# Kernel optimization log

Measured on AMD Instinct MI355X. Metric: run time of the kernel, lower is better.

The kernel has to match this reference:

```python
import jax, jax.numpy as jnp
import numpy as np

EMBED = 768
HIDDEN = 4 * EMBED
TEMPERATURE = 1.0
LN_EPS = 1e-5


def setup_inputs() -> dict:
    key = jax.random.key(0)
    ks = jax.random.split(key, 10)
    s = 1.0 / np.sqrt(EMBED)
    sh = 1.0 / np.sqrt(HIDDEN)
    return {
        "x": jax.random.normal(ks[0], (32, 577, EMBED), dtype=jnp.float32),
        "Wq": jax.random.normal(ks[1], (EMBED, EMBED), dtype=jnp.float32) * s,
        "Wk": jax.random.normal(ks[2], (EMBED, EMBED), dtype=jnp.float32) * s,
        "Wv": jax.random.normal(ks[3], (EMBED, EMBED), dtype=jnp.float32) * s,
        "ln1_g": jnp.ones((EMBED,), jnp.float32),
        "ln1_b": jnp.zeros((EMBED,), jnp.float32),
        "ln2_g": jnp.ones((EMBED,), jnp.float32),
        "ln2_b": jnp.zeros((EMBED,), jnp.float32),
        "W1": jax.random.normal(ks[4], (EMBED, HIDDEN), dtype=jnp.float32) * s,
        "b1": jnp.zeros((HIDDEN,), jnp.float32),
        "W2": jax.random.normal(ks[5], (HIDDEN, EMBED), dtype=jnp.float32) * sh,
        "b2": jnp.zeros((EMBED,), jnp.float32),
    }


def layer_norm(x, g, b):
    mu = jnp.mean(x, axis=-1, keepdims=True)
    var = jnp.mean(jnp.square(x - mu), axis=-1, keepdims=True)
    return (x - mu) * jax.lax.rsqrt(var + LN_EPS) * g + b


def l2_attention(h, Wq, Wk, Wv):
    # h: [b, s, d]
    Q = h @ Wq
    K = h @ Wk
    V = h @ Wv
    q_sq = jnp.sum(Q * Q, axis=-1, keepdims=True)          # [b, s, 1]
    k_sq = jnp.sum(K * K, axis=-1, keepdims=True)          # [b, s, 1]
    qk = jnp.einsum('bqd,bkd->bqk', Q, K)                  # [b, s, s]
    l2_sq = q_sq + jnp.swapaxes(k_sq, -2, -1) - 2.0 * qk
    attn = jax.nn.softmax(-l2_sq / TEMPERATURE, axis=-1)
    return jnp.einsum('bqk,bkd->bqd', attn, V)


def reference(x, Wq, Wk, Wv, ln1_g, ln1_b, ln2_g, ln2_b, W1, b1, W2, b2):
    x = x + l2_attention(layer_norm(x, ln1_g, ln1_b), Wq, Wk, Wv)
    h = layer_norm(x, ln2_g, ln2_b)
    h = jax.nn.gelu(h @ W1 + b1, approximate=False) @ W2 + b2
    return x + h
```

## Files before the change

### kernel.cpp

```cpp
#include <hip/hip_runtime.h>

#define EMBED 768
#define HIDDEN 3072
#define SEQ 577
#define BATCH 32
#define ROWS (BATCH*SEQ)
#define KPAD 608
#define SLD 640

typedef __attribute__((ext_vector_type(4))) float f32x4;
typedef __attribute__((ext_vector_type(8))) __bf16 bf16x8;
typedef unsigned int __attribute__((address_space(1))) as1_u32;
typedef unsigned int __attribute__((address_space(3))) as3_u32;

__device__ __forceinline__ unsigned short f2b(float f) {
    unsigned int u = __float_as_uint(f);
    u = u + 0x7FFFu + ((u >> 16) & 1u);
    return (unsigned short)(u >> 16);
}
__device__ __forceinline__ float b2f(unsigned short s) {
    return __uint_as_float(((unsigned int)s) << 16);
}
__device__ __forceinline__ void gld16(const unsigned short* g, unsigned short* l) {
    __builtin_amdgcn_global_load_lds((const as1_u32*)g, (as3_u32*)l, 16, 0, 0);
}
__device__ __forceinline__ float gelu_f(float x) {
    float u = x * (0.7978845608028654f + 0.03567740814183f * x * x);
    float e = __expf(2.0f * u);
    float th = 1.0f - 2.0f / (e + 1.0f);
    return 0.5f * x * (1.0f + th);
}

__device__ __forceinline__ int swz_lin() {
    int nx = gridDim.x;
    int lin = blockIdx.y * nx + blockIdx.x;
    if (gridDim.z == 1) {
        int nwg = nx * gridDim.y;
        int q = nwg >> 3, r = nwg & 7;
        int xcd = lin & 7, blk = lin >> 3;
        lin = (xcd < r ? xcd * (q + 1) : r * (q + 1) + (xcd - r) * q) + blk;
    }
    return lin;
}

__global__ void ln_kernel(const float* __restrict__ x, const float* __restrict__ g,
                          const float* __restrict__ b, unsigned short* __restrict__ o) {
    int row = blockIdx.x;
    const float* xr = x + (size_t)row * EMBED;
    int t = threadIdx.x;
    float v0 = xr[t], v1 = xr[t + 256], v2 = xr[t + 512];
    float s = v0 + v1 + v2;
    float ss = v0 * v0 + v1 * v1 + v2 * v2;
#pragma unroll
    for (int d = 32; d; d >>= 1) { s += __shfl_down(s, d); ss += __shfl_down(ss, d); }
    __shared__ float rs[4], rss[4];
    if ((t & 63) == 0) { rs[t >> 6] = s; rss[t >> 6] = ss; }
    __syncthreads();
    s = rs[0] + rs[1] + rs[2] + rs[3];
    ss = rss[0] + rss[1] + rss[2] + rss[3];
    float mu = s * (1.0f / EMBED);
    float var = ss * (1.0f / EMBED) - mu * mu;
    float rstd = rsqrtf(var + 1e-5f);
    unsigned short* orow = o + (size_t)row * EMBED;
    orow[t]       = f2b((v0 - mu) * rstd * g[t]       + b[t]);
    orow[t + 256] = f2b((v1 - mu) * rstd * g[t + 256] + b[t + 256]);
    orow[t + 512] = f2b((v2 - mu) * rstd * g[t + 512] + b[t + 512]);
}

__global__ void ln_split_kernel(const float* __restrict__ x, const float* __restrict__ g,
                                const float* __restrict__ b, unsigned short* __restrict__ oh,
                                unsigned short* __restrict__ ol) {
    int row = blockIdx.x;
    const float* xr = x + (size_t)row * EMBED;
    int t = threadIdx.x;
    float v0 = xr[t], v1 = xr[t + 256], v2 = xr[t + 512];
    float s = v0 + v1 + v2;
    float ss = v0 * v0 + v1 * v1 + v2 * v2;
#pragma unroll
    for (int d = 32; d; d >>= 1) { s += __shfl_down(s, d); ss += __shfl_down(ss, d); }
    __shared__ float rs[4], rss[4];
    if ((t & 63) == 0) { rs[t >> 6] = s; rss[t >> 6] = ss; }
    __syncthreads();
    s = rs[0] + rs[1] + rs[2] + rs[3];
    ss = rss[0] + rss[1] + rss[2] + rss[3];
    float mu = s * (1.0f / EMBED);
    float var = ss * (1.0f / EMBED) - mu * mu;
    float rstd = rsqrtf(var + 1e-5f);
    size_t base = (size_t)row * EMBED;
#pragma unroll
    for (int i = 0; i < 3; i++) {
        int d = t + 256 * i;
        float v = (i == 0 ? v0 : (i == 1 ? v1 : v2));
        float y = (v - mu) * rstd * g[d] + b[d];
        unsigned short h = f2b(y);
        oh[base + d] = h;
        ol[base + d] = f2b(y - b2f(h));
    }
}

__global__ void ksq_kernel(const unsigned short* __restrict__ qh,
                           const unsigned short* __restrict__ ql, float* __restrict__ ksq) {
    int row = blockIdx.x;
    int t = threadIdx.x;
    size_t base = (size_t)row * 1536 + EMBED;
    float s = 0.f;
#pragma unroll
    for (int i = 0; i < 3; i++) {
        int d = t + 256 * i;
        float k = b2f(qh[base + d]) + b2f(ql[base + d]);
        s += k * k;
    }
#pragma unroll
    for (int d = 32; d; d >>= 1) s += __shfl_down(s, d);
    __shared__ float rs[4];
    if ((t & 63) == 0) rs[t >> 6] = s;
    __syncthreads();
    if (t == 0) ksq[row] = rs[0] + rs[1] + rs[2] + rs[3];
}

__global__ void softmax_kernel(const float* __restrict__ S, unsigned short* __restrict__ P) {
    int r = blockIdx.x;
    int t = threadIdx.x;
    const float* sr = S + (size_t)r * SLD;
    float v0 = sr[t];
    float v1 = sr[t + 256];
    float v2 = (t + 512 < SEQ) ? sr[t + 512] : -3.0e38f;
    float m = fmaxf(v0, fmaxf(v1, v2));
#pragma unroll
    for (int d = 32; d; d >>= 1) m = fmaxf(m, __shfl_down(m, d));
    __shared__ float rm[4];
    if ((t & 63) == 0) rm[t >> 6] = m;
    __syncthreads();
    m = fmaxf(fmaxf(rm[0], rm[1]), fmaxf(rm[2], rm[3]));
    float e0 = __expf(v0 - m);
    float e1 = __expf(v1 - m);
    float e2 = (t + 512 < SEQ) ? __expf(v2 - m) : 0.0f;
    float s = e0 + e1 + e2;
#pragma unroll
    for (int d = 32; d; d >>= 1) s += __shfl_down(s, d);
    __shared__ float rsum[4];
    if ((t & 63) == 0) rsum[t >> 6] = s;
    __syncthreads();
    float inv = 1.0f / (rsum[0] + rsum[1] + rsum[2] + rsum[3]);
    unsigned short* pr = P + (size_t)r * KPAD;
    pr[t]       = f2b(e0 * inv);
    pr[t + 256] = f2b(e1 * inv);
    if (t + 512 < KPAD) pr[t + 512] = f2b(e2 * inv);
}

__global__ void wt_kernel(const float* __restrict__ in, unsigned short* __restrict__ out,
                          int K, int N, int outRowOff, int outLd) {
    __shared__ float tile[32][33];
    int n0 = blockIdx.x * 32, k0 = blockIdx.y * 32;
    int tx = threadIdx.x, ty = threadIdx.y;
#pragma unroll
    for (int i = 0; i < 4; i++)
        tile[ty + 8 * i][tx] = in[(size_t)(k0 + ty + 8 * i) * N + (n0 + tx)];
    __syncthreads();
#pragma unroll
    for (int i = 0; i < 4; i++)
        out[(size_t)(outRowOff + n0 + ty + 8 * i) * outLd + (k0 + tx)] = f2b(tile[tx][ty + 8 * i]);
}

__global__ void wt_split2_kernel(const float* __restrict__ Wq, const float* __restrict__ Wk,
                                 unsigned short* __restrict__ oh, unsigned short* __restrict__ ol) {
    const float* in = blockIdx.z ? Wk : Wq;
    int outRowOff = blockIdx.z * EMBED;
    __shared__ float tile[32][33];
    int n0 = blockIdx.x * 32, k0 = blockIdx.y * 32;
    int tx = threadIdx.x, ty = threadIdx.y;
#pragma unroll
    for (int i = 0; i < 4; i++)
        tile[ty + 8 * i][tx] = in[(size_t)(k0 + ty + 8 * i) * EMBED + (n0 + tx)];
    __syncthreads();
#pragma unroll
    for (int i = 0; i < 4; i++) {
        float v = tile[tx][ty + 8 * i];
        unsigned short h = f2b(v);
        size_t idx = (size_t)(outRowOff + n0 + ty + 8 * i) * EMBED + (k0 + tx);
        oh[idx] = h;
        ol[idx] = f2b(v - b2f(h));
    }
}

__global__ void vt_kernel(const unsigned short* __restrict__ vbuf, unsigned short* __restrict__ vt) {
    int z = blockIdx.z;
    int d0 = blockIdx.x * 32, c0 = blockIdx.y * 32;
    __shared__ unsigned short tile[32][33];
    int tx = threadIdx.x, ty = threadIdx.y;
#pragma unroll
    for (int i = 0; i < 4; i++) {
        int c = c0 + ty + 8 * i;
        tile[ty + 8 * i][tx] = (c < SEQ) ? vbuf[((size_t)z * SEQ + c) * EMBED + d0 + tx]
                                         : (unsigned short)0;
    }
    __syncthreads();
#pragma unroll
    for (int i = 0; i < 4; i++) {
        int d = d0 + 8 * i + ty, c = c0 + tx;
        vt[(size_t)z * EMBED * KPAD + (size_t)d * KPAD + c] = tile[tx][ty + 8 * i];
    }
}

template <int EPI>
__global__ __launch_bounds__(256, 2) void gemm_bt(
    const unsigned short* __restrict__ A, int lda, long long sA,
    const unsigned short* __restrict__ B, int ldb, long long sB,
    int M, int N, int K,
    void* __restrict__ C, int ldc, long long sC,
    const float* __restrict__ E, long long sE) {
    __shared__ unsigned short As[3][4096];
    __shared__ unsigned short Bs[3][4096];
    int z = blockIdx.z;
    A += (size_t)z * sA;
    B += (size_t)z * sB;
    int nx = gridDim.x;
    int lin = swz_lin();
    int row0 = (lin / nx) * 128, col0 = (lin % nx) * 128;
    int t = threadIdx.x, l = t & 63, w = t >> 6;
    int wr = w >> 1, wc = w & 1;
    int l15 = l & 15, kb = l >> 4;

    f32x4 acc[4][4] = {};

    int srow = t >> 2;
    int kboff = ((t & 3) ^ ((srow >> 1) & 3)) * 8;

    int aoE[2], boE[2];
#pragma unroll
    for (int c = 0; c < 2; ++c) {
        int ar = row0 + c * 64 + srow; ar = ar < M ? ar : M - 1;
        aoE[c] = ar * lda + kboff;
        int br = col0 + c * 64 + srow; br = br < N ? br : N - 1;
        boE[c] = br * ldb + kboff;
    }
    int aoff[4], boff[4];
#pragma unroll
    for (int m = 0; m < 4; m++) {
        int r = wr * 64 + m * 16 + l15;
        aoff[m] = r * 32 + (kb ^ ((r >> 1) & 3)) * 8;
        int rn = wc * 64 + m * 16 + l15;
        boff[m] = rn * 32 + (kb ^ ((rn >> 1) & 3)) * 8;
    }

    auto compute = [&](int sl) {
        bf16x8 af[4], bfr[4];
#pragma unroll
        for (int m = 0; m < 4; m++) af[m] = *reinterpret_cast<const bf16x8*>(&As[sl][aoff[m]]);
#pragma unroll
        for (int n = 0; n < 4; n++) bfr[n] = *reinterpret_cast<const bf16x8*>(&Bs[sl][boff[n]]);
#pragma unroll
        for (int m = 0; m < 4; m++)
#pragma unroll
            for (int n = 0; n < 4; n++)
                acc[m][n] = __builtin_amdgcn_mfma_f32_16x16x32_bf16(af[m], bfr[n], acc[m][n], 0, 0, 0);
    };

    int ldsoff = t * 8;
    for (int kt = 0; kt < K; kt += 96) {
#pragma unroll
        for (int s = 0; s < 3; ++s) {
            int ks = kt + 32 * s;
            if (ks < K) {
                gld16(A + (size_t)(aoE[0] + ks), &As[s][ldsoff]);
                gld16(A + (size_t)(aoE[1] + ks), &As[s][2048 + ldsoff]);
                gld16(B + (size_t)(boE[0] + ks), &Bs[s][ldsoff]);
                gld16(B + (size_t)(boE[1] + ks), &Bs[s][2048 + ldsoff]);
            }
        }
        asm volatile("s_waitcnt vmcnt(0)" ::: "memory");
        __builtin_amdgcn_s_barrier();
        __builtin_amdgcn_sched_barrier(0);
#pragma unroll
        for (int s = 0; s < 3; ++s)
            if (kt + 32 * s < K) compute(s);
        __builtin_amdgcn_s_barrier();
        __builtin_amdgcn_sched_barrier(0);
    }

    int rbase = row0 + wr * 64 + (l >> 4) * 4;
    int cbase = col0 + wc * 64 + l15;
    auto epi = [&](bool chk) {
#pragma unroll
        for (int m = 0; m < 4; m++) {
#pragma unroll
            for (int n = 0; n < 4; n++) {
                int col = cbase + n * 16;
                if (chk && col >= N) continue;
#pragma unroll
                for (int j = 0; j < 4; j++) {
                    int row = rbase + m * 16 + j;
                    if (chk && row >= M) continue;
                    float v = acc[m][n][j];
                    size_t oidx = (size_t)z * sC + (size_t)row * ldc + col;
                    if (EPI == 0) {
                        ((unsigned short*)C)[oidx] = f2b(v);
                    } else if (EPI == 2) {
                        ((float*)C)[oidx] = E[oidx] + v;
                    } else if (EPI == 3) {
                        ((unsigned short*)C)[oidx] = f2b(gelu_f(v + E[col]));
                    } else if (EPI == 4) {
                        ((float*)C)[oidx] += v + E[col];
                    }
                }
            }
        }
    };
    if (row0 + 128 <= M && col0 + 128 <= N) epi(false); else epi(true);
}

template <int EPI>
__global__ __launch_bounds__(256, 2) void gemm_hp(
    const unsigned short* __restrict__ Ah, const unsigned short* __restrict__ Al, int lda, long long sA,
    const unsigned short* __restrict__ Bh, const unsigned short* __restrict__ Bl, int ldb, long long sB,
    int M, int N, int K,
    void* __restrict__ C, int ldc, long long sC, long long planeOff,
    const float* __restrict__ E, long long sE) {
    __shared__ unsigned short Ash[4096], Asl[4096], Bsh[4096], Bsl[4096];
    int z = blockIdx.z;
    Ah += (size_t)z * sA; Al += (size_t)z * sA;
    Bh += (size_t)z * sB; Bl += (size_t)z * sB;
    int nx = gridDim.x;
    int lin = swz_lin();
    int row0 = (lin / nx) * 128, col0 = (lin % nx) * 128;
    int t = threadIdx.x, l = t & 63, w = t >> 6;
    int wr = w >> 1, wc = w & 1;
    int l15 = l & 15, kb = l >> 4;

    f32x4 acc[4][4] = {};

    int srow = t >> 2;
    int kboff = ((t & 3) ^ ((srow >> 1) & 3)) * 8;

    int aoE[2], boE[2];
#pragma unroll
    for (int c = 0; c < 2; ++c) {
        int ar = row0 + c * 64 + srow; ar = ar < M ? ar : M - 1;
        aoE[c] = ar * lda + kboff;
        int br = col0 + c * 64 + srow; br = br < N ? br : N - 1;
        boE[c] = br * ldb + kboff;
    }
    int aoff[4], boff[4];
#pragma unroll
    for (int m = 0; m < 4; m++) {
        int r = wr * 64 + m * 16 + l15;
        aoff[m] = r * 32 + (kb ^ ((r >> 1) & 3)) * 8;
        int rn = wc * 64 + m * 16 + l15;
        boff[m] = rn * 32 + (kb ^ ((rn >> 1) & 3)) * 8;
    }

    int ldsoff = t * 8;
    for (int kt = 0; kt < K; kt += 32) {
#pragma unroll
        for (int c = 0; c < 2; ++c) {
            gld16(Ah + (size_t)(aoE[c] + kt), &Ash[c * 2048 + ldsoff]);
            gld16(Al + (size_t)(aoE[c] + kt), &Asl[c * 2048 + ldsoff]);
            gld16(Bh + (size_t)(boE[c] + kt), &Bsh[c * 2048 + ldsoff]);
            gld16(Bl + (size_t)(boE[c] + kt), &Bsl[c * 2048 + ldsoff]);
        }
        __syncthreads();
        bf16x8 afh[4], afl[4], bfh[4], bfl[4];
#pragma unroll
        for (int m = 0; m < 4; m++) {
            afh[m] = *reinterpret_cast<const bf16x8*>(&Ash[aoff[m]]);
            afl[m] = *reinterpret_cast<const bf16x8*>(&Asl[aoff[m]]);
        }
#pragma unroll
        for (int n = 0; n < 4; n++) {
            bfh[n] = *reinterpret_cast<const bf16x8*>(&Bsh[boff[n]]);
            bfl[n] = *reinterpret_cast<const bf16x8*>(&Bsl[boff[n]]);
        }
#pragma unroll
        for (int m = 0; m < 4; m++)
#pragma unroll
            for (int n = 0; n < 4; n++) {
                acc[m][n] = __builtin_amdgcn_mfma_f32_16x16x32_bf16(afh[m], bfh[n], acc[m][n], 0, 0, 0);
                acc[m][n] = __builtin_amdgcn_mfma_f32_16x16x32_bf16(afh[m], bfl[n], acc[m][n], 0, 0, 0);
                acc[m][n] = __builtin_amdgcn_mfma_f32_16x16x32_bf16(afl[m], bfh[n], acc[m][n], 0, 0, 0);
            }
        __syncthreads();
    }

    int rbase = row0 + wr * 64 + (l >> 4) * 4;
    int cbase = col0 + wc * 64 + l15;
    auto epi = [&](bool chk) {
#pragma unroll
        for (int m = 0; m < 4; m++) {
#pragma unroll
            for (int n = 0; n < 4; n++) {
                int col = cbase + n * 16;
                if (chk && col >= N) continue;
#pragma unroll
                for (int j = 0; j < 4; j++) {
                    int row = rbase + m * 16 + j;
                    if (chk && row >= M) continue;
                    float v = acc[m][n][j];
                    size_t oidx = (size_t)z * sC + (size_t)row * ldc + col;
                    if (EPI == 0) {
                        unsigned short h = f2b(v);
                        ((unsigned short*)C)[oidx] = h;
                        ((unsigned short*)C)[oidx + planeOff] = f2b(v - b2f(h));
                    } else if (EPI == 1) {
                        ((float*)C)[oidx] = 2.0f * v - E[(size_t)z * sE + col];
                    }
                }
            }
        }
    };
    if (row0 + 128 <= M && col0 + 128 <= N) epi(false); else epi(true);
}

extern "C" void kernel_launch(void* const* d_in, const int* in_sizes, int n_in,
                              void* d_out, int out_size, void* d_ws, size_t ws_size,
                              hipStream_t stream) {
    const float* x   = (const float*)d_in[0];
    const float* Wq  = (const float*)d_in[1];
    const float* Wk  = (const float*)d_in[2];
    const float* Wv  = (const float*)d_in[3];
    const float* g1  = (const float*)d_in[4];
    const float* be1 = (const float*)d_in[5];
    const float* g2  = (const float*)d_in[6];
    const float* be2 = (const float*)d_in[7];
    const float* W1  = (const float*)d_in[8];
    const float* bb1 = (const float*)d_in[9];
    const float* W2  = (const float*)d_in[10];
    const float* bb2 = (const float*)d_in[11];
    float* out = (float*)d_out;

    char* ws = (char*)d_ws;
    size_t off = 0;
    auto alloc = [&](size_t bytes) -> char* {
        char* p = ws + off;
        off += (bytes + 255) & ~(size_t)255;
        return p;
    };
    unsigned short* wqkTh = (unsigned short*)alloc((size_t)1536 * EMBED * 2);
    unsigned short* wqkTl = (unsigned short*)alloc((size_t)1536 * EMBED * 2);
    unsigned short* wvT   = (unsigned short*)alloc((size_t)EMBED * EMBED * 2);
    unsigned short* w1T   = (unsigned short*)alloc((size_t)HIDDEN * EMBED * 2);
    unsigned short* w2T   = (unsigned short*)alloc((size_t)EMBED * HIDDEN * 2);
    float*          ksqb  = (float*)alloc((size_t)ROWS * 4);
    char* regB = alloc((size_t)ROWS * HIDDEN * 2);
    char* regC = alloc((size_t)2 * ROWS * EMBED * 2);
    unsigned short* vbuf  = (unsigned short*)alloc((size_t)ROWS * EMBED * 2);
    unsigned short* vtb   = (unsigned short*)alloc((size_t)BATCH * EMBED * KPAD * 2);
    unsigned short* Pbuf  = (unsigned short*)alloc((size_t)ROWS * KPAD * 2);
    if (off > ws_size) return;

    unsigned short* qkh  = (unsigned short*)regB;
    unsigned short* qkl  = qkh + (size_t)ROWS * 1536;
    unsigned short* hid  = (unsigned short*)regB;
    unsigned short* h1h  = (unsigned short*)regC;
    unsigned short* h1l  = h1h + (size_t)ROWS * EMBED;
    float*          Sbuf = (float*)regC;
    unsigned short* h2   = (unsigned short*)regC;

    dim3 b256(256), bT(32, 8);

    wt_split2_kernel<<<dim3(24, 24, 2), bT, 0, stream>>>(Wq, Wk, wqkTh, wqkTl);
    wt_kernel<<<dim3(24, 24), bT, 0, stream>>>(Wv, wvT, EMBED, EMBED, 0, EMBED);
    wt_kernel<<<dim3(96, 24), bT, 0, stream>>>(W1, w1T, EMBED, HIDDEN, 0, EMBED);
    wt_kernel<<<dim3(24, 96), bT, 0, stream>>>(W2, w2T, HIDDEN, EMBED, 0, HIDDEN);

    ln_split_kernel<<<ROWS, b256, 0, stream>>>(x, g1, be1, h1h, h1l);

    gemm_hp<0><<<dim3(12, 145, 1), b256, 0, stream>>>(
        h1h, h1l, EMBED, 0, wqkTh, wqkTl, EMBED, 0,
        ROWS, 1536, EMBED, qkh, 1536, 0, (long long)ROWS * 1536, nullptr, 0);

    gemm_bt<0><<<dim3(6, 145, 1), b256, 0, stream>>>(
        h1h, EMBED, 0, wvT, EMBED, 0, ROWS, EMBED, EMBED, vbuf, EMBED, 0, nullptr, 0);

    ksq_kernel<<<ROWS, b256, 0, stream>>>(qkh, qkl, ksqb);

    gemm_hp<1><<<dim3(5, 5, 32), b256, 0, stream>>>(
        qkh, qkl, 1536, (long long)SEQ * 1536, qkh + EMBED, qkl + EMBED, 1536, (long long)SEQ * 1536,
        SEQ, SEQ, EMBED, Sbuf, SLD, (long long)SEQ * SLD, 0, ksqb, SEQ);

    softmax_kernel<<<ROWS, b256, 0, stream>>>(Sbuf, Pbuf);

    vt_kernel<<<dim3(24, 19, 32), bT, 0, stream>>>(vbuf, vtb);

    gemm_bt<2><<<dim3(6, 5, 32), b256, 0, stream>>>(
        Pbuf, KPAD, (long long)SEQ * KPAD, vtb, KPAD, (long long)EMBED * KPAD,
        SEQ, EMBED, KPAD, out, EMBED, (long long)SEQ * EMBED, x, (long long)SEQ * EMBED);

    ln_kernel<<<ROWS, b256, 0, stream>>>(out, g2, be2, h2);

    gemm_bt<3><<<dim3(24, 145, 1), b256, 0, stream>>>(
        h2, EMBED, 0, w1T, EMBED, 0, ROWS, HIDDEN, EMBED, hid, HIDDEN, 0, bb1, 0);

    gemm_bt<4><<<dim3(6, 145, 1), b256, 0, stream>>>(
        hid, HIDDEN, 0, w2T, HIDDEN, 0, ROWS, EMBED, HIDDEN, out, EMBED, 0, bb2, 0);
}
```

Measured before the change: 818.6 us.

## Double-buffer GEMM K-loop with prefetch two stages ahead

Replaces the load-three-stages-then-compute-all loop with a two-slot ring. The load for step u+2 is issued while step u+1's data is already resident, and the wait uses vmcnt(4) so global-to-LDS loads overlap with MFMA compute. Shared memory drops from three slots to two per operand, which may also allow higher occupancy. In exchange it adds two barriers per 32-wide K step and issues redundant clamped loads at the tail.

```diff
diff --git a/kernel.cpp b/kernel.cpp
--- a/kernel.cpp
+++ b/kernel.cpp
@@ -209,8 +209,8 @@
     int M, int N, int K,
     void* __restrict__ C, int ldc, long long sC,
     const float* __restrict__ E, long long sE) {
-    __shared__ unsigned short As[3][4096];
-    __shared__ unsigned short Bs[3][4096];
+    __shared__ unsigned short As[2][4096];
+    __shared__ unsigned short Bs[2][4096];
     int z = blockIdx.z;
     A += (size_t)z * sA;
     B += (size_t)z * sB;
@@ -243,6 +243,13 @@
         boff[m] = rn * 32 + (kb ^ ((rn >> 1) & 3)) * 8;
     }
 
+    int ldsoff = t * 8;
+    auto stage = [&](int sl, int kt) {
+        gld16(A + (size_t)(aoE[0] + kt), &As[sl][ldsoff]);
+        gld16(A + (size_t)(aoE[1] + kt), &As[sl][2048 + ldsoff]);
+        gld16(B + (size_t)(boE[0] + kt), &Bs[sl][ldsoff]);
+        gld16(B + (size_t)(boE[1] + kt), &Bs[sl][2048 + ldsoff]);
+    };
     auto compute = [&](int sl) {
         bf16x8 af[4], bfr[4];
 #pragma unroll
@@ -256,27 +263,22 @@
                 acc[m][n] = __builtin_amdgcn_mfma_f32_16x16x32_bf16(af[m], bfr[n], acc[m][n], 0, 0, 0);
     };
 
-    int ldsoff = t * 8;
-    for (int kt = 0; kt < K; kt += 96) {
-#pragma unroll
-        for (int s = 0; s < 3; ++s) {
-            int ks = kt + 32 * s;
-            if (ks < K) {
-                gld16(A + (size_t)(aoE[0] + ks), &As[s][ldsoff]);
-                gld16(A + (size_t)(aoE[1] + ks), &As[s][2048 + ldsoff]);
-                gld16(B + (size_t)(boE[0] + ks), &Bs[s][ldsoff]);
-                gld16(B + (size_t)(boE[1] + ks), &Bs[s][2048 + ldsoff]);
-            }
-        }
-        asm volatile("s_waitcnt vmcnt(0)" ::: "memory");
+    int NW = K >> 5;
+    stage(0, 0);
+    stage(1, 32);
+    asm volatile("s_waitcnt vmcnt(4)" ::: "memory");
+    __builtin_amdgcn_s_barrier();
+    __builtin_amdgcn_sched_barrier(0);
+    for (int u = 0; u < NW; ++u) {
+        compute(u & 1);
+        __builtin_amdgcn_s_barrier();
+        int kn = (u + 2 < NW ? u + 2 : NW - 1) << 5;
+        stage(u & 1, kn);
+        asm volatile("s_waitcnt vmcnt(4)" ::: "memory");
         __builtin_amdgcn_s_barrier();
         __builtin_amdgcn_sched_barrier(0);
-#pragma unroll
-        for (int s = 0; s < 3; ++s)
-            if (kt + 32 * s < K) compute(s);
-        __builtin_amdgcn_s_barrier();
-        __builtin_amdgcn_sched_barrier(0);
-    }
+    }
+    asm volatile("s_waitcnt vmcnt(0)" ::: "memory");
 
     int rbase = row0 + wr * 64 + (l >> 4) * 4;
     int cbase = col0 + wc * 64 + l15;
```

After: 800.5 us. 1.02x faster.

## Enlarge GEMM block tiles to 256x128 with 512-thread blocks

Applied to the files above, without the earlier changes.

Both GEMM kernels now use 512 threads (8 waves) per block, and each block computes a 256x128 output tile instead of 128x128, so every B tile loaded into LDS is reused across twice as many rows. gemm_bt moves from a 3-stage K batch of 96 to a 2-stage batch of 64 so LDS stays the same size, and all launch grids are halved in the row dimension. The aim is less global traffic and fewer blocks overall. In exchange there are fewer blocks to spread over the CUs, per-CU register pressure rises, and more work is wasted on the padded last tile for the 577-row batched GEMMs.

```diff
diff --git a/kernel.cpp b/kernel.cpp
--- a/kernel.cpp
+++ b/kernel.cpp
@@ -203,20 +203,20 @@
 }
 
 template <int EPI>
-__global__ __launch_bounds__(256, 2) void gemm_bt(
+__global__ __launch_bounds__(512, 2) void gemm_bt(
     const unsigned short* __restrict__ A, int lda, long long sA,
     const unsigned short* __restrict__ B, int ldb, long long sB,
     int M, int N, int K,
     void* __restrict__ C, int ldc, long long sC,
     const float* __restrict__ E, long long sE) {
-    __shared__ unsigned short As[3][4096];
-    __shared__ unsigned short Bs[3][4096];
+    __shared__ unsigned short As[2][8192];
+    __shared__ unsigned short Bs[2][4096];
     int z = blockIdx.z;
     A += (size_t)z * sA;
     B += (size_t)z * sB;
     int nx = gridDim.x;
     int lin = swz_lin();
-    int row0 = (lin / nx) * 128, col0 = (lin % nx) * 128;
+    int row0 = (lin / nx) * 256, col0 = (lin % nx) * 128;
     int t = threadIdx.x, l = t & 63, w = t >> 6;
     int wr = w >> 1, wc = w & 1;
     int l15 = l & 15, kb = l >> 4;
@@ -226,13 +226,15 @@
     int srow = t >> 2;
     int kboff = ((t & 3) ^ ((srow >> 1) & 3)) * 8;
 
-    int aoE[2], boE[2];
+    int aoE[2], boE;
 #pragma unroll
     for (int c = 0; c < 2; ++c) {
-        int ar = row0 + c * 64 + srow; ar = ar < M ? ar : M - 1;
+        int ar = row0 + c * 128 + srow; ar = ar < M ? ar : M - 1;
         aoE[c] = ar * lda + kboff;
-        int br = col0 + c * 64 + srow; br = br < N ? br : N - 1;
-        boE[c] = br * ldb + kboff;
+    }
+    {
+        int br = col0 + srow; br = br < N ? br : N - 1;
+        boE = br * ldb + kboff;
     }
     int aoff[4], boff[4];
 #pragma unroll
@@ -257,23 +259,21 @@
     };
 
     int ldsoff = t * 8;
-    for (int kt = 0; kt < K; kt += 96) {
-#pragma unroll
-        for (int s = 0; s < 3; ++s) {
-            int ks = kt + 32 * s;
-            if (ks < K) {
-                gld16(A + (size_t)(aoE[0] + ks), &As[s][ldsoff]);
-                gld16(A + (size_t)(aoE[1] + ks), &As[s][2048 + ldsoff]);
-                gld16(B + (size_t)(boE[0] + ks), &Bs[s][ldsoff]);
-                gld16(B + (size_t)(boE[1] + ks), &Bs[s][2048 + ldsoff]);
-            }
+    for (int kt = 0; kt < K; kt += 64) {
+        gld16(A + (size_t)(aoE[0] + kt), &As[0][ldsoff]);
+        gld16(A + (size_t)(aoE[1] + kt), &As[0][4096 + ldsoff]);
+        gld16(B + (size_t)(boE + kt), &Bs[0][ldsoff]);
+        bool has2 = (kt + 32) < K;
+        if (has2) {
+            gld16(A + (size_t)(aoE[0] + kt + 32), &As[1][ldsoff]);
+            gld16(A + (size_t)(aoE[1] + kt + 32), &As[1][4096 + ldsoff]);
+            gld16(B + (size_t)(boE + kt + 32), &Bs[1][ldsoff]);
         }
         asm volatile("s_waitcnt vmcnt(0)" ::: "memory");
         __builtin_amdgcn_s_barrier();
         __builtin_amdgcn_sched_barrier(0);
-#pragma unroll
-        for (int s = 0; s < 3; ++s)
-            if (kt + 32 * s < K) compute(s);
+        compute(0);
+        if (has2) compute(1);
         __builtin_amdgcn_s_barrier();
         __builtin_amdgcn_sched_barrier(0);
     }
@@ -306,23 +306,23 @@
             }
         }
     };
-    if (row0 + 128 <= M && col0 + 128 <= N) epi(false); else epi(true);
+    if (row0 + 256 <= M && col0 + 128 <= N) epi(false); else epi(true);
 }
 
 template <int EPI>
-__global__ __launch_bounds__(256, 2) void gemm_hp(
+__global__ __launch_bounds__(512, 2) void gemm_hp(
     const unsigned short* __restrict__ Ah, const unsigned short* __restrict__ Al, int lda, long long sA,
     const unsigned short* __restrict__ Bh, const unsigned short* __restrict__ Bl, int ldb, long long sB,
     int M, int N, int K,
     void* __restrict__ C, int ldc, long long sC, long long planeOff,
     const float* __restrict__ E, long long sE) {
-    __shared__ unsigned short Ash[4096], Asl[4096], Bsh[4096], Bsl[4096];
+    __shared__ unsigned short Ash[8192], Asl[8192], Bsh[4096], Bsl[4096];
     int z = blockIdx.z;
     Ah += (size_t)z * sA; Al += (size_t)z * sA;
     Bh += (size_t)z * sB; Bl += (size_t)z * sB;
     int nx = gridDim.x;
     int lin = swz_lin();
-    int row0 = (lin / nx) * 128, col0 = (lin % nx) * 128;
+    int row0 = (lin / nx) * 256, col0 = (lin % nx) * 128;
     int t = threadIdx.x, l = t & 63, w = t >> 6;
     int wr = w >> 1, wc = w & 1;
     int l15 = l & 15, kb = l >> 4;
@@ -332,13 +332,15 @@
     int srow = t >> 2;
     int kboff = ((t & 3) ^ ((srow >> 1) & 3)) * 8;
 
-    int aoE[2], boE[2];
+    int aoE[2], boE;
 #pragma unroll
     for (int c = 0; c < 2; ++c) {
-        int ar = row0 + c * 64 + srow; ar = ar < M ? ar : M - 1;
+        int ar = row0 + c * 128 + srow; ar = ar < M ? ar : M - 1;
         aoE[c] = ar * lda + kboff;
-        int br = col0 + c * 64 + srow; br = br < N ? br : N - 1;
-        boE[c] = br * ldb + kboff;
+    }
+    {
+        int br = col0 + srow; br = br < N ? br : N - 1;
+        boE = br * ldb + kboff;
     }
     int aoff[4], boff[4];
 #pragma unroll
@@ -351,13 +353,12 @@
 
     int ldsoff = t * 8;
     for (int kt = 0; kt < K; kt += 32) {
-#pragma unroll
-        for (int c = 0; c < 2; ++c) {
-            gld16(Ah + (size_t)(aoE[c] + kt), &Ash[c * 2048 + ldsoff]);
-            gld16(Al + (size_t)(aoE[c] + kt), &Asl[c * 2048 + ldsoff]);
-            gld16(Bh + (size_t)(boE[c] + kt), &Bsh[c * 2048 + ldsoff]);
-            gld16(Bl + (size_t)(boE[c] + kt), &Bsl[c * 2048 + ldsoff]);
-        }
+        gld16(Ah + (size_t)(aoE[0] + kt), &Ash[ldsoff]);
+        gld16(Ah + (size_t)(aoE[1] + kt), &Ash[4096 + ldsoff]);
+        gld16(Al + (size_t)(aoE[0] + kt), &Asl[ldsoff]);
+        gld16(Al + (size_t)(aoE[1] + kt), &Asl[4096 + ldsoff]);
+        gld16(Bh + (size_t)(boE + kt), &Bsh[ldsoff]);
+        gld16(Bl + (size_t)(boE + kt), &Bsl[ldsoff]);
         __syncthreads();
         bf16x8 afh[4], afl[4], bfh[4], bfl[4];
 #pragma unroll
@@ -407,7 +408,7 @@
             }
         }
     };
-    if (row0 + 128 <= M && col0 + 128 <= N) epi(false); else epi(true);
+    if (row0 + 256 <= M && col0 + 128 <= N) epi(false); else epi(true);
 }
 
 extern "C" void kernel_launch(void* const* d_in, const int* in_sizes, int n_in,
@@ -455,7 +456,7 @@
     float*          Sbuf = (float*)regC;
     unsigned short* h2   = (unsigned short*)regC;
 
-    dim3 b256(256), bT(32, 8);
+    dim3 b256(256), b512(512), bT(32, 8);
 
     wt_split2_kernel<<<dim3(24, 24, 2), bT, 0, stream>>>(Wq, Wk, wqkTh, wqkTl);
     wt_kernel<<<dim3(24, 24), bT, 0, stream>>>(Wv, wvT, EMBED, EMBED, 0, EMBED);
@@ -464,16 +465,16 @@
 
     ln_split_kernel<<<ROWS, b256, 0, stream>>>(x, g1, be1, h1h, h1l);
 
-    gemm_hp<0><<<dim3(12, 145, 1), b256, 0, stream>>>(
+    gemm_hp<0><<<dim3(12, 73, 1), b512, 0, stream>>>(
         h1h, h1l, EMBED, 0, wqkTh, wqkTl, EMBED, 0,
         ROWS, 1536, EMBED, qkh, 1536, 0, (long long)ROWS * 1536, nullptr, 0);
 
-    gemm_bt<0><<<dim3(6, 145, 1), b256, 0, stream>>>(
+    gemm_bt<0><<<dim3(6, 73, 1), b512, 0, stream>>>(
         h1h, EMBED, 0, wvT, EMBED, 0, ROWS, EMBED, EMBED, vbuf, EMBED, 0, nullptr, 0);
 
     ksq_kernel<<<ROWS, b256, 0, stream>>>(qkh, qkl, ksqb);
 
-    gemm_hp<1><<<dim3(5, 5, 32), b256, 0, stream>>>(
+    gemm_hp<1><<<dim3(5, 3, 32), b512, 0, stream>>>(
         qkh, qkl, 1536, (long long)SEQ * 1536, qkh + EMBED, qkl + EMBED, 1536, (long long)SEQ * 1536,
         SEQ, SEQ, EMBED, Sbuf, SLD, (long long)SEQ * SLD, 0, ksqb, SEQ);
 
@@ -481,15 +482,15 @@
 
     vt_kernel<<<dim3(24, 19, 32), bT, 0, stream>>>(vbuf, vtb);
 
-    gemm_bt<2><<<dim3(6, 5, 32), b256, 0, stream>>>(
+    gemm_bt<2><<<dim3(6, 3, 32), b512, 0, stream>>>(
         Pbuf, KPAD, (long long)SEQ * KPAD, vtb, KPAD, (long long)EMBED * KPAD,
         SEQ, EMBED, KPAD, out, EMBED, (long long)SEQ * EMBED, x, (long long)SEQ * EMBED);
 
     ln_kernel<<<ROWS, b256, 0, stream>>>(out, g2, be2, h2);
 
-    gemm_bt<3><<<dim3(24, 145, 1), b256, 0, stream>>>(
+    gemm_bt<3><<<dim3(24, 73, 1), b512, 0, stream>>>(
         h2, EMBED, 0, w1T, EMBED, 0, ROWS, HIDDEN, EMBED, hid, HIDDEN, 0, bb1, 0);
 
-    gemm_bt<4><<<dim3(6, 145, 1), b256, 0, stream>>>(
+    gemm_bt<4><<<dim3(6, 73, 1), b512, 0, stream>>>(
         hid, HIDDEN, 0, w2T, HIDDEN, 0, ROWS, EMBED, HIDDEN, out, EMBED, 0, bb2, 0);
 }
```

New measurement: 737.0 us. -10.0%, faster.

## Load B fragments directly from global into registers, shrink LDS staging

Applied to the files above, without the earlier changes.

Both GEMM kernels stop staging the B operand through shared memory and instead have each lane load its B fragments straight from global memory into registers. Only A is staged in LDS, so the LDS footprint drops and the launch bound is raised to three blocks per CU. The bt kernel also cuts its per-iteration K stage from three to two. The cost is uncoalesced, redundant global loads of B across waves, with no reuse through LDS. The column bounds check in the epilogue is removed, so N must be a multiple of 128.

```diff
diff --git a/kernel.cpp b/kernel.cpp
--- a/kernel.cpp
+++ b/kernel.cpp
@@ -203,14 +203,13 @@
 }
 
 template <int EPI>
-__global__ __launch_bounds__(256, 2) void gemm_bt(
+__global__ __launch_bounds__(256, 3) void gemm_bt(
     const unsigned short* __restrict__ A, int lda, long long sA,
     const unsigned short* __restrict__ B, int ldb, long long sB,
     int M, int N, int K,
     void* __restrict__ C, int ldc, long long sC,
     const float* __restrict__ E, long long sE) {
-    __shared__ unsigned short As[3][4096];
-    __shared__ unsigned short Bs[3][4096];
+    __shared__ unsigned short As[2][4096];
     int z = blockIdx.z;
     A += (size_t)z * sA;
     B += (size_t)z * sB;
@@ -226,29 +225,27 @@
     int srow = t >> 2;
     int kboff = ((t & 3) ^ ((srow >> 1) & 3)) * 8;
 
-    int aoE[2], boE[2];
+    int aoE[2];
 #pragma unroll
     for (int c = 0; c < 2; ++c) {
         int ar = row0 + c * 64 + srow; ar = ar < M ? ar : M - 1;
         aoE[c] = ar * lda + kboff;
-        int br = col0 + c * 64 + srow; br = br < N ? br : N - 1;
-        boE[c] = br * ldb + kboff;
-    }
-    int aoff[4], boff[4];
+    }
+    int aoff[4];
 #pragma unroll
     for (int m = 0; m < 4; m++) {
         int r = wr * 64 + m * 16 + l15;
         aoff[m] = r * 32 + (kb ^ ((r >> 1) & 3)) * 8;
-        int rn = wc * 64 + m * 16 + l15;
-        boff[m] = rn * 32 + (kb ^ ((rn >> 1) & 3)) * 8;
-    }
-
-    auto compute = [&](int sl) {
-        bf16x8 af[4], bfr[4];
+    }
+    int boG[4];
+#pragma unroll
+    for (int n = 0; n < 4; n++)
+        boG[n] = (col0 + wc * 64 + n * 16 + l15) * ldb + kb * 8;
+
+    auto compute = [&](int sl, const bf16x8* bfr) {
+        bf16x8 af[4];
 #pragma unroll
         for (int m = 0; m < 4; m++) af[m] = *reinterpret_cast<const bf16x8*>(&As[sl][aoff[m]]);
-#pragma unroll
-        for (int n = 0; n < 4; n++) bfr[n] = *reinterpret_cast<const bf16x8*>(&Bs[sl][boff[n]]);
 #pragma unroll
         for (int m = 0; m < 4; m++)
 #pragma unroll
@@ -257,23 +254,28 @@
     };
 
     int ldsoff = t * 8;
-    for (int kt = 0; kt < K; kt += 96) {
-#pragma unroll
-        for (int s = 0; s < 3; ++s) {
-            int ks = kt + 32 * s;
-            if (ks < K) {
-                gld16(A + (size_t)(aoE[0] + ks), &As[s][ldsoff]);
-                gld16(A + (size_t)(aoE[1] + ks), &As[s][2048 + ldsoff]);
-                gld16(B + (size_t)(boE[0] + ks), &Bs[s][ldsoff]);
-                gld16(B + (size_t)(boE[1] + ks), &Bs[s][2048 + ldsoff]);
-            }
+    for (int kt = 0; kt < K; kt += 64) {
+        gld16(A + (size_t)(aoE[0] + kt), &As[0][ldsoff]);
+        gld16(A + (size_t)(aoE[1] + kt), &As[0][2048 + ldsoff]);
+        bool has2 = (kt + 32) < K;
+        if (has2) {
+            gld16(A + (size_t)(aoE[0] + kt + 32), &As[1][ldsoff]);
+            gld16(A + (size_t)(aoE[1] + kt + 32), &As[1][2048 + ldsoff]);
+        }
+        bf16x8 bf0[4], bf1[4];
+#pragma unroll
+        for (int n = 0; n < 4; n++)
+            bf0[n] = *reinterpret_cast<const bf16x8*>(B + (size_t)(boG[n] + kt));
+        if (has2) {
+#pragma unroll
+            for (int n = 0; n < 4; n++)
+                bf1[n] = *reinterpret_cast<const bf16x8*>(B + (size_t)(boG[n] + kt + 32));
         }
         asm volatile("s_waitcnt vmcnt(0)" ::: "memory");
         __builtin_amdgcn_s_barrier();
         __builtin_amdgcn_sched_barrier(0);
-#pragma unroll
-        for (int s = 0; s < 3; ++s)
-            if (kt + 32 * s < K) compute(s);
+        compute(0, bf0);
+        if (has2) compute(1, bf1);
         __builtin_amdgcn_s_barrier();
         __builtin_amdgcn_sched_barrier(0);
     }
@@ -286,7 +288,6 @@
 #pragma unroll
             for (int n = 0; n < 4; n++) {
                 int col = cbase + n * 16;
-                if (chk && col >= N) continue;
 #pragma unroll
                 for (int j = 0; j < 4; j++) {
                     int row = rbase + m * 16 + j;
@@ -306,17 +307,17 @@
             }
         }
     };
-    if (row0 + 128 <= M && col0 + 128 <= N) epi(false); else epi(true);
+    if (row0 + 128 <= M) epi(false); else epi(true);
 }
 
 template <int EPI>
-__global__ __launch_bounds__(256, 2) void gemm_hp(
+__global__ __launch_bounds__(256, 3) void gemm_hp(
     const unsigned short* __restrict__ Ah, const unsigned short* __restrict__ Al, int lda, long long sA,
     const unsigned short* __restrict__ Bh, const unsigned short* __restrict__ Bl, int ldb, long long sB,
     int M, int N, int K,
     void* __restrict__ C, int ldc, long long sC, long long planeOff,
     const float* __restrict__ E, long long sE) {
-    __shared__ unsigned short Ash[4096], Asl[4096], Bsh[4096], Bsl[4096];
+    __shared__ unsigned short Ash[4096], Asl[4096];
     int z = blockIdx.z;
     Ah += (size_t)z * sA; Al += (size_t)z * sA;
     Bh += (size_t)z * sB; Bl += (size_t)z * sB;
@@ -332,43 +333,43 @@
     int srow = t >> 2;
     int kboff = ((t & 3) ^ ((srow >> 1) & 3)) * 8;
 
-    int aoE[2], boE[2];
+    int aoE[2];
 #pragma unroll
     for (int c = 0; c < 2; ++c) {
         int ar = row0 + c * 64 + srow; ar = ar < M ? ar : M - 1;
         aoE[c] = ar * lda + kboff;
-        int br = col0 + c * 64 + srow; br = br < N ? br : N - 1;
-        boE[c] = br * ldb + kboff;
-    }
-    int aoff[4], boff[4];
+    }
+    int aoff[4];
 #pragma unroll
     for (int m = 0; m < 4; m++) {
         int r = wr * 64 + m * 16 + l15;
         aoff[m] = r * 32 + (kb ^ ((r >> 1) & 3)) * 8;
-        int rn = wc * 64 + m * 16 + l15;
-        boff[m] = rn * 32 + (kb ^ ((rn >> 1) & 3)) * 8;
-    }
+    }
+    int boG[4];
+#pragma unroll
+    for (int n = 0; n < 4; n++)
+        boG[n] = (col0 + wc * 64 + n * 16 + l15) * ldb + kb * 8;
 
     int ldsoff = t * 8;
     for (int kt = 0; kt < K; kt += 32) {
-#pragma unroll
-        for (int c = 0; c < 2; ++c) {
-            gld16(Ah + (size_t)(aoE[c] + kt), &Ash[c * 2048 + ldsoff]);
-            gld16(Al + (size_t)(aoE[c] + kt), &Asl[c * 2048 + ldsoff]);
-            gld16(Bh + (size_t)(boE[c] + kt), &Bsh[c * 2048 + ldsoff]);
-            gld16(Bl + (size_t)(boE[c] + kt), &Bsl[c * 2048 + ldsoff]);
-        }
-        __syncthreads();
-        bf16x8 afh[4], afl[4], bfh[4], bfl[4];
+        gld16(Ah + (size_t)(aoE[0] + kt), &Ash[ldsoff]);
+        gld16(Ah + (size_t)(aoE[1] + kt), &Ash[2048 + ldsoff]);
+        gld16(Al + (size_t)(aoE[0] + kt), &Asl[ldsoff]);
+        gld16(Al + (size_t)(aoE[1] + kt), &Asl[2048 + ldsoff]);
+        bf16x8 bfh[4], bfl[4];
+#pragma unroll
+        for (int n = 0; n < 4; n++) {
+            bfh[n] = *reinterpret_cast<const bf16x8*>(Bh + (size_t)(boG[n] + kt));
+            bfl[n] = *reinterpret_cast<const bf16x8*>(Bl + (size_t)(boG[n] + kt));
+        }
+        asm volatile("s_waitcnt vmcnt(0)" ::: "memory");
+        __builtin_amdgcn_s_barrier();
+        __builtin_amdgcn_sched_barrier(0);
+        bf16x8 afh[4], afl[4];
 #pragma unroll
         for (int m = 0; m < 4; m++) {
             afh[m] = *reinterpret_cast<const bf16x8*>(&Ash[aoff[m]]);
             afl[m] = *reinterpret_cast<const bf16x8*>(&Asl[aoff[m]]);
-        }
-#pragma unroll
-        for (int n = 0; n < 4; n++) {
-            bfh[n] = *reinterpret_cast<const bf16x8*>(&Bsh[boff[n]]);
-            bfl[n] = *reinterpret_cast<const bf16x8*>(&Bsl[boff[n]]);
         }
 #pragma unroll
         for (int m = 0; m < 4; m++)
@@ -378,7 +379,8 @@
                 acc[m][n] = __builtin_amdgcn_mfma_f32_16x16x32_bf16(afh[m], bfl[n], acc[m][n], 0, 0, 0);
                 acc[m][n] = __builtin_amdgcn_mfma_f32_16x16x32_bf16(afl[m], bfh[n], acc[m][n], 0, 0, 0);
             }
-        __syncthreads();
+        __builtin_amdgcn_s_barrier();
+        __builtin_amdgcn_sched_barrier(0);
     }
 
     int rbase = row0 + wr * 64 + (l >> 4) * 4;
```

Measured after the change: 1.060 ms. 1.3x slower.
